# Performance work log

Hardware: AMD Instinct MI355X
Metric: run time of the kernel (lower is better)

Reference implementation:

```python
import jax, jax.numpy as jnp
import numpy as np

B, L, D, H = 2, 4096, 1024, 4
DK = D // H
DV = D // H
CHUNK, FIRS, FIRL, CONV, GROUP = 32, 3, 31, 4, 2
EPS_ID, R_EPS = 0.06, 0.025   # step==0 -> router epsilon at its start value
R_HID = 2 * D
R_IN = D + H * 6


def _l2norm(x, eps=1e-6):
    return x * jax.lax.rsqrt(jnp.sum(x * x, -1, keepdims=True) + eps)


def _causal_dwconv(x, w):
    # x: (b, l, c), w: (c, k); depthwise causal conv1d
    c = x.shape[-1]
    k = w.shape[-1]
    lhs = jnp.swapaxes(x, 1, 2)              # (b, c, l)
    rhs = w[:, None, :]                      # (c, 1, k)
    y = jax.lax.conv_general_dilated(lhs, rhs, window_strides=(1,), padding=[(k - 1, 0)],
                                     dimension_numbers=('NCH', 'OIH', 'NCH'), feature_group_count=c)
    return jnp.swapaxes(y, 1, 2)


def _fir(x, filt):
    # x: (b, l, h, d), filt: (h, d, k) depthwise causal FIR per head-channel
    b, l, h, d = x.shape
    y = _causal_dwconv(x.reshape(b, l, h * d), filt.reshape(h * d, -1))
    return y.reshape(b, l, h, d)


def _delta_rule_chunkwise(q, k, v, beta, chunk=CHUNK):
    # q,k: (b,h,L,dk)  v: (b,h,L,dv)  beta: (b,h,L); L % chunk == 0
    b, h, Ls, dk = q.shape
    dv = v.shape[-1]
    n = Ls // chunk
    q = _l2norm(q)
    k = _l2norm(k)
    v = v * beta[..., None]
    kb = k * beta[..., None]
    rs = lambda t: t.reshape(b, h, n, chunk, -1)
    q, k, v, kb = map(rs, (q, k, v, kb))
    tri = jnp.triu(jnp.ones((chunk, chunk), bool), 0)
    # UT transform: forward substitution to invert (I + strictly-lower(K_beta K^T))
    T = jnp.where(tri, 0.0, -(kb @ jnp.swapaxes(k, -1, -2)))
    for i in range(1, chunk):
        T = T.at[..., i, :].add(jnp.einsum('...j,...jl->...l', T[..., i, :], T))
    T = T + jnp.eye(chunk, dtype=T.dtype)
    u = T @ v          # (b,h,n,c,dv)
    w = T @ kb         # (b,h,n,c,dk)
    fmask = jnp.triu(jnp.ones((chunk, chunk), bool), 1)
    mv = lambda t: jnp.moveaxis(t, 2, 0)

    def step(S, xs):
        qi, ki, ui, wi = xs
        attn = jnp.where(fmask, 0.0, qi @ jnp.swapaxes(ki, -1, -2))
        u2 = ui - wi @ S
        oi = qi @ S + attn @ u2
        return S + jnp.swapaxes(ki, -1, -2) @ u2, oi

    S0 = jnp.zeros((b, h, dk, dv), q.dtype)
    S, o = jax.lax.scan(step, S0, (mv(q), mv(k), mv(u), mv(w)))
    return jnp.moveaxis(o, 0, 2).reshape(b, h, Ls, dv), S


def setup_inputs():
    key = jax.random.key(0)
    ks = jax.random.split(key, 20)
    lin = lambda kk, i, o: 0.02 * jax.random.normal(kk, (i, o), jnp.float32)

    def fir(kk, kern):
        base = jnp.zeros((H, DV, kern), jnp.float32).at[:, :, -1].set(1.0)
        return base + 0.01 * jax.random.normal(kk, (H, DV, kern), jnp.float32)

    return {
        'hidden_states': jax.random.normal(ks[0], (B, L, D), jnp.float32),
        'Wq': lin(ks[1], D, H * DK), 'Wk': lin(ks[2], D, H * DK), 'Wv': lin(ks[3], D, H * DV),
        'Wb': lin(ks[4], D, H),
        'conv_q': 0.3 * jax.random.normal(ks[5], (H * DK, CONV), jnp.float32),
        'conv_k': 0.3 * jax.random.normal(ks[6], (H * DK, CONV), jnp.float32),
        'conv_v': 0.3 * jax.random.normal(ks[7], (H * DV, CONV), jnp.float32),
        'fir_short': fir(ks[8], FIRS), 'fir_long': fir(ks[9], FIRL),
        'alpha_id': jnp.zeros((H,), jnp.float32),
        'Wid': lin(ks[10], D, H), 'bid': jnp.zeros((H,), jnp.float32),
        'Wr1': lin(ks[11], R_IN, R_HID), 'br1': jnp.zeros((R_HID,), jnp.float32),
        'Wr2': lin(ks[12], R_HID, H * 3), 'br2': jnp.zeros((H * 3,), jnp.float32),
        'log_tau_group': jnp.zeros(((H + GROUP - 1) // GROUP,), jnp.float32),
        'log_tau_head': jnp.zeros((H,), jnp.float32),
        'o_norm_w': jnp.ones((DV,), jnp.float32),
        'Wo': lin(ks[13], H * DV, D),
    }


def reference(hidden_states, Wq, Wk, Wv, Wb, conv_q, conv_k, conv_v, fir_short, fir_long,
              alpha_id, Wid, bid, Wr1, br1, Wr2, br2, log_tau_group, log_tau_head, o_norm_w, Wo):
    x = hidden_states
    b, l = x.shape[:2]
    # projections + causal short conv + silu (qk_activation='silu')
    q = jax.nn.silu(_causal_dwconv(x @ Wq, conv_q))
    k = jax.nn.silu(_causal_dwconv(x @ Wk, conv_k))
    v = jax.nn.silu(_causal_dwconv(x @ Wv, conv_v))
    qh = q.reshape(b, l, H, DK)
    kh = k.reshape(b, l, H, DK)
    vh = v.reshape(b, l, H, DV)
    beta = jax.nn.sigmoid(x @ Wb)                      # (b,l,h)
    bhld = lambda t: jnp.transpose(t, (0, 2, 1, 3))
    delta, _S = _delta_rule_chunkwise(bhld(qh), bhld(kh), bhld(vh), jnp.transpose(beta, (0, 2, 1)))
    delta = jnp.transpose(delta, (0, 2, 1, 3))         # (b,l,h,dv)
    fs = _fir(vh, fir_short)
    fl = _fir(vh, fir_long)
    # per-head mean/std stats of the three branch outputs
    stats = jnp.concatenate([fs.mean(-1), fs.std(-1), fl.mean(-1), fl.std(-1),
                             delta.mean(-1), delta.std(-1)], -1)   # (b,l,6h)
    router_in = jnp.concatenate([x, stats], -1)
    hmid = jax.nn.gelu(router_in @ Wr1 + br1, approximate=False)
    logits = (hmid @ Wr2 + br2).reshape(b, l, H, 3)
    group_idx = jnp.arange(H) // GROUP
    # step==0 -> mix=1.0: tau is the per-group temperature
    tau = jnp.exp(log_tau_group)[group_idx] + 0.0 * jnp.exp(log_tau_head)
    p = jax.nn.softmax(logits / tau[None, None, :, None], -1)
    p = p * (1.0 - 3.0 * R_EPS) + R_EPS                # epsilon-floor
    o = p[..., 0:1] * fs + p[..., 1:2] * fl + p[..., 2:3] * delta
    # gated identity (value) path
    id_scale = EPS_ID + jax.nn.sigmoid(alpha_id)[None, None, :] * jax.nn.sigmoid(x @ Wid + bid)
    o = o + id_scale[..., None] * vh
    # per-head RMSNorm then output projection
    o = o * jax.lax.rsqrt(jnp.mean(o * o, -1, keepdims=True) + 1e-5) * o_norm_w
    return o.reshape(b, l, H * DV) @ Wo
```

## Files before the change

### kernel.cpp

```cpp
#include <hip/hip_runtime.h>
#include <hip/hip_bf16.h>
#include <math.h>

#define BATCH 2
#define SEQ 4096
#define DMODEL 1024
#define NH 4
#define DHEAD 256
#define NCHUNK 128
#define ROWS (BATCH * SEQ)

typedef short s8v __attribute__((ext_vector_type(8)));
typedef float f4v __attribute__((ext_vector_type(4)));

__device__ __forceinline__ float sigm(float x) { return 1.0f / (1.0f + expf(-x)); }
__device__ __forceinline__ float siluf(float x) { return x / (1.0f + expf(-x)); }
__device__ __forceinline__ unsigned short f2b(float f) {
  __hip_bfloat16 h = __float2bfloat16(f);
  return *(unsigned short*)&h;
}
__device__ __forceinline__ float b2f(unsigned short u) {
  __hip_bfloat16 h = *(__hip_bfloat16*)&u;
  return __bfloat162float(h);
}

__global__ __launch_bounds__(256) void prep_x(
    const float* __restrict__ x, __hip_bfloat16* __restrict__ xb,
    const float* __restrict__ Wb, const float* __restrict__ Wid,
    const float* __restrict__ alpha_id, const float* __restrict__ bidp,
    float* __restrict__ beta, float* __restrict__ idsc) {
  const int row = blockIdx.x;
  const int t = threadIdx.x;
  const long base = (long)row * DMODEL + t * 4;
  float4 xv = *(const float4*)(x + base);
  {
    __hip_bfloat16 tmp[4] = {__float2bfloat16(xv.x), __float2bfloat16(xv.y),
                             __float2bfloat16(xv.z), __float2bfloat16(xv.w)};
    *(ushort4*)(xb + base) = *(ushort4*)tmp;
  }
  float xa[4] = {xv.x, xv.y, xv.z, xv.w};
  float ab[4] = {0, 0, 0, 0}, ai[4] = {0, 0, 0, 0};
#pragma unroll
  for (int i = 0; i < 4; ++i) {
    int k = t * 4 + i;
    float4 wb4 = *(const float4*)(Wb + k * 4);
    float4 wi4 = *(const float4*)(Wid + k * 4);
    ab[0] = fmaf(xa[i], wb4.x, ab[0]); ab[1] = fmaf(xa[i], wb4.y, ab[1]);
    ab[2] = fmaf(xa[i], wb4.z, ab[2]); ab[3] = fmaf(xa[i], wb4.w, ab[3]);
    ai[0] = fmaf(xa[i], wi4.x, ai[0]); ai[1] = fmaf(xa[i], wi4.y, ai[1]);
    ai[2] = fmaf(xa[i], wi4.z, ai[2]); ai[3] = fmaf(xa[i], wi4.w, ai[3]);
  }
#pragma unroll
  for (int m = 1; m < 64; m <<= 1) {
#pragma unroll
    for (int hh = 0; hh < 4; ++hh) {
      ab[hh] += __shfl_xor(ab[hh], m);
      ai[hh] += __shfl_xor(ai[hh], m);
    }
  }
  __shared__ float red[4][8];
  if ((t & 63) == 0) {
    int wv = t >> 6;
#pragma unroll
    for (int hh = 0; hh < 4; ++hh) {
      red[wv][hh] = ab[hh];
      red[wv][4 + hh] = ai[hh];
    }
  }
  __syncthreads();
  if (t < 8) {
    float s = red[0][t] + red[1][t] + red[2][t] + red[3][t];
    if (t < 4) {
      beta[(long)row * NH + t] = sigm(s);
    } else {
      int hh = t - 4;
      idsc[(long)row * NH + hh] = 0.06f + sigm(alpha_id[hh]) * sigm(s + bidp[hh]);
    }
  }
}

__global__ __launch_bounds__(256) void transpose_cast(
    const float* __restrict__ W, __hip_bfloat16* __restrict__ Wt,
    int K, int N, int Ks) {
  __shared__ float tile[32][33];
  const int t = threadIdx.x;
  const int tx = t & 31, ty = t >> 5;
  const int kb = blockIdx.y * 32, nb = blockIdx.x * 32;
#pragma unroll
  for (int r = 0; r < 4; ++r) {
    int kk = kb + ty + 8 * r;
    tile[ty + 8 * r][tx] = (kk < K) ? W[(long)kk * N + nb + tx] : 0.f;
  }
  __syncthreads();
#pragma unroll
  for (int r = 0; r < 4; ++r) {
    Wt[(long)(nb + ty + 8 * r) * Ks + kb + tx] = __float2bfloat16(tile[tx][ty + 8 * r]);
  }
}

__global__ __launch_bounds__(256) void fir_transpose(
    const float* __restrict__ fshort, const float* __restrict__ flong,
    float* __restrict__ fsT, float* __restrict__ flT) {
  const int j = blockIdx.x;
  const int t = threadIdx.x;
  if (j < 31) {
#pragma unroll
    for (int i = 0; i < 4; ++i) {
      int c = t * 4 + i;
      flT[j * 1024 + c] = flong[c * 31 + j];
    }
  } else {
    int tp = j - 31;
#pragma unroll
    for (int i = 0; i < 4; ++i) {
      int c = t * 4 + i;
      fsT[tp * 1024 + c] = fshort[c * 3 + tp];
    }
  }
}

template <int ACT, bool BF16OUT>
__global__ __launch_bounds__(256) void gemm_bf16(
    const __hip_bfloat16* __restrict__ A, const __hip_bfloat16* __restrict__ Bt,
    const float* __restrict__ bias, void* __restrict__ Cv,
    int M, int N, int Ks) {
  __shared__ short As[128 * 32];
  __shared__ short Bs[128 * 32];
  const int t = threadIdx.x;
  const int wv = t >> 6;
  const int lane = t & 63;
  const int row0 = blockIdx.y * 128, col0 = blockIdx.x * 128;
  const int mq = (wv >> 1) * 64, nq = (wv & 1) * 64;
  const int ln15 = lane & 15;
  const int kq = (lane >> 4) * 8;
  const int sr = t >> 2;
  const int sc = (t & 3) * 8;
  const short* Ag = (const short*)A + (long)(row0 + sr) * Ks + sc;
  const short* Bg = (const short*)Bt + (long)(col0 + sr) * Ks + sc;
  const long rstep = (long)64 * Ks;

  f4v acc[4][4];
#pragma unroll
  for (int i = 0; i < 4; ++i)
#pragma unroll
    for (int j = 0; j < 4; ++j) acc[i][j] = (f4v){0.f, 0.f, 0.f, 0.f};

  uint4 a0 = *(const uint4*)(Ag);
  uint4 a1 = *(const uint4*)(Ag + rstep);
  uint4 b0 = *(const uint4*)(Bg);
  uint4 b1 = *(const uint4*)(Bg + rstep);
// ... 216 lines not shown
#pragma unroll
    for (int i = 0; i < 32; ++i) acc[i] = 0.f;
    for (int j = 0; j < 32; ++j) {
      float vv = v[((long)(b * SEQ + l0 + j)) * DMODEL + h * DHEAD + d];
#pragma unroll
      for (int i = 0; i < 32; ++i) acc[i] = fmaf(T[i][j], vv, acc[i]);
    }
    long ubase = ((long)bh * SEQ + l0) * DHEAD + d;
#pragma unroll
    for (int i = 0; i < 32; ++i) u[ubase + (long)i * DHEAD] = acc[i];
#pragma unroll
    for (int i = 0; i < 32; ++i) acc[i] = 0.f;
    for (int j = 0; j < 32; ++j) {
      float kv = b2f((unsigned short)khi[j * 264 + d]) + b2f((unsigned short)klo[j * 264 + d]);
#pragma unroll
      for (int i = 0; i < 32; ++i) acc[i] = fmaf(T[i][j], kv, acc[i]);
    }
#pragma unroll
    for (int i = 0; i < 32; ++i) wb16[ubase + (long)i * DHEAD] = __float2bfloat16(acc[i]);
  }

  {
    const int s = t;
    unsigned short* kb = (unsigned short*)kTb16 + ((long)bh * NCHUNK + c) * 8192 + (long)s * 32;
#pragma unroll
    for (int i4 = 0; i4 < 8; ++i4) {
      ushort4 pk;
      pk.x = (unsigned short)khi[(i4 * 4 + 0) * 264 + s];
      pk.y = (unsigned short)khi[(i4 * 4 + 1) * 264 + s];
      pk.z = (unsigned short)khi[(i4 * 4 + 2) * 264 + s];
      pk.w = (unsigned short)khi[(i4 * 4 + 3) * 264 + s];
      *(ushort4*)(kb + i4 * 4) = pk;
    }
  }
}

__global__ __launch_bounds__(64, 1) void phaseB(
    const __hip_bfloat16* __restrict__ qpk,
    const __hip_bfloat16* __restrict__ wb,
    const __hip_bfloat16* __restrict__ kTb,
    const __hip_bfloat16* __restrict__ attnb,
    const float* __restrict__ u, float* __restrict__ delta ) {
  __shared__ __align__(16) short St[16 * 264];
  __shared__ __align__(16) short Ut[16 * 40];
  const int bid = blockIdx.x;
  const int slice = bid & 15;
  const int bh = bid >> 4;
  const int d0 = slice * 16;
  const int t = threadIdx.x;
  const int ln15 = t & 15;
  const int qw = t >> 4;

  const short* wbase = (const short*)wb + (long)bh * SEQ * 256;
  const short* qbase = (const short*)qpk + (long)bh * SEQ * 256;
  const short* kTbase = (const short*)kTb + (long)bh * NCHUNK * 8192;
  const short* atbase = (const short*)attnb + (long)bh * NCHUNK * 1024;
  const float* ubase = u + (long)bh * SEQ * 256;
  float* dbase = delta + (long)bh * SEQ * 256;

  f4v Sacc[16];
#pragma unroll
  for (int kt = 0; kt < 16; ++kt) Sacc[kt] = (f4v){0.f, 0.f, 0.f, 0.f};

  s8v wA[2][8], kA[16], atv[2];
  float uf[2][4];
  {
#pragma unroll
    for (int mt = 0; mt < 2; ++mt)
#pragma unroll
      for (int ks = 0; ks < 8; ++ks)
        wA[mt][ks] = *(const s8v*)(wbase + (long)(mt * 16 + ln15) * 256 + ks * 32 + qw * 8);
#pragma unroll
    for (int kt = 0; kt < 16; ++kt)
      kA[kt] = *(const s8v*)(kTbase + (kt * 16 + ln15) * 32 + qw * 8);
#pragma unroll
    for (int mt = 0; mt < 2; ++mt) {
      atv[mt] = *(const s8v*)(atbase + (mt * 16 + ln15) * 32 + qw * 8);
#pragma unroll
      for (int r = 0; r < 4; ++r)
        uf[mt][r] = ubase[(long)(mt * 16 + qw * 4 + r) * 256 + d0 + ln15];
    }
  }

  for (int c = 0; c < NCHUNK; ++c) {
    const int l0 = c * 32;

    s8v qA[2][8];
#pragma unroll
    for (int mt = 0; mt < 2; ++mt)
#pragma unroll
      for (int ks = 0; ks < 8; ++ks)
        qA[mt][ks] = *(const s8v*)(qbase + (long)(l0 + mt * 16 + ln15) * 256 + ks * 32 + qw * 8);

#pragma unroll
    for (int kt = 0; kt < 16; ++kt) {
      ushort4 pk;
      pk.x = f2b(Sacc[kt][0]); pk.y = f2b(Sacc[kt][1]);
      pk.z = f2b(Sacc[kt][2]); pk.w = f2b(Sacc[kt][3]);
      *(ushort4*)&St[ln15 * 264 + kt * 16 + qw * 4] = pk;
    }
    asm volatile("s_waitcnt lgkmcnt(0)" ::: "memory");
    s8v bS[8];
#pragma unroll
    for (int ks = 0; ks < 8; ++ks)
      bS[ks] = *(const s8v*)&St[ln15 * 264 + ks * 32 + qw * 8];

    f4v dwa0 = (f4v){0.f,0.f,0.f,0.f}, dwb0 = (f4v){0.f,0.f,0.f,0.f};
    f4v dwa1 = (f4v){0.f,0.f,0.f,0.f}, dwb1 = (f4v){0.f,0.f,0.f,0.f};
#pragma unroll
    for (int ks = 0; ks < 4; ++ks) {
      dwa0 = __builtin_amdgcn_mfma_f32_16x16x32_bf16(wA[0][ks], bS[ks], dwa0, 0, 0, 0);
      dwa1 = __builtin_amdgcn_mfma_f32_16x16x32_bf16(wA[1][ks], bS[ks], dwa1, 0, 0, 0);
      dwb0 = __builtin_amdgcn_mfma_f32_16x16x32_bf16(wA[0][ks + 4], bS[ks + 4], dwb0, 0, 0, 0);
      dwb1 = __builtin_amdgcn_mfma_f32_16x16x32_bf16(wA[1][ks + 4], bS[ks + 4], dwb1, 0, 0, 0);
    }
    float u2a[4], u2b[4];
#pragma unroll
    for (int r = 0; r < 4; ++r) {
      u2a[r] = uf[0][r] - (dwa0[r] + dwb0[r]);
      u2b[r] = uf[1][r] - (dwa1[r] + dwb1[r]);
    }
    {
      ushort4 pa, pb;
      pa.x = f2b(u2a[0]); pa.y = f2b(u2a[1]); pa.z = f2b(u2a[2]); pa.w = f2b(u2a[3]);
      pb.x = f2b(u2b[0]); pb.y = f2b(u2b[1]); pb.z = f2b(u2b[2]); pb.w = f2b(u2b[3]);
      *(ushort4*)&Ut[ln15 * 40 + qw * 4] = pa;
      *(ushort4*)&Ut[ln15 * 40 + 16 + qw * 4] = pb;
    }
    asm volatile("s_waitcnt lgkmcnt(0)" ::: "memory");
    s8v bu = *(const s8v*)&Ut[ln15 * 40 + qw * 8];

    f4v oA0 = __builtin_amdgcn_mfma_f32_16x16x32_bf16(atv[0], bu, (f4v){0.f,0.f,0.f,0.f}, 0, 0, 0);
    f4v oA1 = __builtin_amdgcn_mfma_f32_16x16x32_bf16(atv[1], bu, (f4v){0.f,0.f,0.f,0.f}, 0, 0, 0);

#pragma unroll
    for (int kt = 0; kt < 16; ++kt)
      Sacc[kt] = __builtin_amdgcn_mfma_f32_16x16x32_bf16(kA[kt], bu, Sacc[kt], 0, 0, 0);

    if (c + 1 < NCHUNK) {
      const int ln = l0 + 32;
#pragma unroll
      for (int mt = 0; mt < 2; ++mt)
#pragma unroll
        for (int ks = 0; ks < 8; ++ks)
          wA[mt][ks] = *(const s8v*)(wbase + (long)(ln + mt * 16 + ln15) * 256 + ks * 32 + qw * 8);
#pragma unroll
      for (int kt = 0; kt < 16; ++kt)
        kA[kt] = *(const s8v*)(kTbase + (long)(c + 1) * 8192 + (kt * 16 + ln15) * 32 + qw * 8);
#pragma unroll
      for (int mt = 0; mt < 2; ++mt) {
        atv[mt] = *(const s8v*)(atbase + (long)(c + 1) * 1024 + (mt * 16 + ln15) * 32 + qw * 8);
#pragma unroll
        for (int r = 0; r < 4; ++r)
          uf[mt][r] = ubase[(long)(ln + mt * 16 + qw * 4 + r) * 256 + d0 + ln15];
      }
    }

    f4v oB0 = (f4v){0.f,0.f,0.f,0.f}, oB1 = (f4v){0.f,0.f,0.f,0.f};
#pragma unroll
    for (int ks = 0; ks < 4; ++ks) {
      oA0 = __builtin_amdgcn_mfma_f32_16x16x32_bf16(qA[0][ks], bS[ks], oA0, 0, 0, 0);
      oA1 = __builtin_amdgcn_mfma_f32_16x16x32_bf16(qA[1][ks], bS[ks], oA1, 0, 0, 0);
      oB0 = __builtin_amdgcn_mfma_f32_16x16x32_bf16(qA[0][ks + 4], bS[ks + 4], oB0, 0, 0, 0);
      oB1 = __builtin_amdgcn_mfma_f32_16x16x32_bf16(qA[1][ks + 4], bS[ks + 4], oB1, 0, 0, 0);
    }
#pragma unroll
    for (int r = 0; r < 4; ++r) {
      dbase[(long)(l0 + qw * 4 + r) * 256 + d0 + ln15] = oA0[r] + oB0[r];
      dbase[(long)(l0 + 16 + qw * 4 + r) * 256 + d0 + ln15] = oA1[r] + oB1[r];
    }
  }
}

__global__ __launch_bounds__(256) void fir_kernel(
    const float* __restrict__ v, const float* __restrict__ fsT,
    const float* __restrict__ flT, float* __restrict__ fs, float* __restrict__ fl) {
  const int row = blockIdx.x;
  const int l = row & (SEQ - 1);
  const int t = threadIdx.x;
  const int cb = t * 4;
  float4 accl = make_float4(0, 0, 0, 0);
  float4 accs = make_float4(0, 0, 0, 0);
  const float* vb = v + (long)(row - 30) * DMODEL + cb;
  if (l >= 30) {
#pragma unroll
    for (int j = 0; j < 31; ++j) {
      float4 w4 = *(const float4*)(flT + j * DMODEL + cb);
      float4 xv = *(const float4*)(vb + (long)j * DMODEL);
      accl.x = fmaf(w4.x, xv.x, accl.x);
      accl.y = fmaf(w4.y, xv.y, accl.y);
      accl.z = fmaf(w4.z, xv.z, accl.z);
      accl.w = fmaf(w4.w, xv.w, accl.w);
      if (j >= 28) {
        float4 s4 = *(const float4*)(fsT + (j - 28) * DMODEL + cb);
        accs.x = fmaf(s4.x, xv.x, accs.x);
        accs.y = fmaf(s4.y, xv.y, accs.y);
        accs.z = fmaf(s4.z, xv.z, accs.z);
        accs.w = fmaf(s4.w, xv.w, accs.w);
      }
    }
  } else {
    for (int j = 30 - l; j < 31; ++j) {
      float4 w4 = *(const float4*)(flT + j * DMODEL + cb);
      float4 xv = *(const float4*)(vb + (long)j * DMODEL);
      accl.x = fmaf(w4.x, xv.x, accl.x);
      accl.y = fmaf(w4.y, xv.y, accl.y);
      accl.z = fmaf(w4.z, xv.z, accl.z);
      accl.w = fmaf(w4.w, xv.w, accl.w);
      if (j >= 28) {
        float4 s4 = *(const float4*)(fsT + (j - 28) * DMODEL + cb);
        accs.x = fmaf(s4.x, xv.x, accs.x);
        accs.y = fmaf(s4.y, xv.y, accs.y);
        accs.z = fmaf(s4.z, xv.z, accs.z);
        accs.w = fmaf(s4.w, xv.w, accs.w);
      }
    }
  }
  *(float4*)(fs + (long)row * DMODEL + cb) = accs;
  *(float4*)(fl + (long)row * DMODEL + cb) = accl;
}

__global__ __launch_bounds__(256) void stats_router(
    const float* __restrict__ x, const float* __restrict__ fs,
    const float* __restrict__ fl, const float* __restrict__ dl,
    __hip_bfloat16* __restrict__ rinb) {
  const int row = blockIdx.x;
  const int b = row >> 12;
  const int l = row & (SEQ - 1);
  const int t = threadIdx.x;
  float4 xv = *(const float4*)(x + (long)row * DMODEL + t * 4);
  {
    __hip_bfloat16 tmp[4] = {__float2bfloat16(xv.x), __float2bfloat16(xv.y),
                             __float2bfloat16(xv.z), __float2bfloat16(xv.w)};
    *(ushort4*)(rinb + (long)row * 1056 + t * 4) = *(ushort4*)tmp;
  }
  if (t < 8) rinb[(long)row * 1056 + 1048 + t] = __float2bfloat16(0.f);
  const int h = t >> 6;
  const int lane = t & 63;
  const long base = (long)row * DMODEL + h * DHEAD + lane * 4;
  const long dbase = ((long)(b * NH + h) * SEQ + l) * DHEAD + lane * 4;
  float4 a = *(const float4*)(fs + base);
  float4 bq = *(const float4*)(fl + base);
  float4 cq = *(const float4*)(dl + dbase);
  float s[6];
  s[0] = a.x + a.y + a.z + a.w;
  s[1] = a.x * a.x + a.y * a.y + a.z * a.z + a.w * a.w;
  s[2] = bq.x + bq.y + bq.z + bq.w;
  s[3] = bq.x * bq.x + bq.y * bq.y + bq.z * bq.z + bq.w * bq.w;
  s[4] = cq.x + cq.y + cq.z + cq.w;
  s[5] = cq.x * cq.x + cq.y * cq.y + cq.z * cq.z + cq.w * cq.w;
#pragma unroll
  for (int m = 1; m < 64; m <<= 1)
#pragma unroll
    for (int j = 0; j < 6; ++j) s[j] += __shfl_xor(s[j], m);
  if (lane == 0) {
    __hip_bfloat16* rb = rinb + (long)row * 1056 + 1024;
    float m0 = s[0] * (1.f / 256.f);
    float m1 = s[2] * (1.f / 256.f);
    float m2 = s[4] * (1.f / 256.f);
    rb[h] = __float2bfloat16(m0);
    rb[4 + h] = __float2bfloat16(sqrtf(fmaxf(s[1] * (1.f / 256.f) - m0 * m0, 0.f)));
    rb[8 + h] = __float2bfloat16(m1);
    rb[12 + h] = __float2bfloat16(sqrtf(fmaxf(s[3] * (1.f / 256.f) - m1 * m1, 0.f)));
    rb[16 + h] = __float2bfloat16(m2);
    rb[20 + h] = __float2bfloat16(sqrtf(fmaxf(s[5] * (1.f / 256.f) - m2 * m2, 0.f)));
  }
}

__global__ __launch_bounds__(256) void router_logits(
    const __hip_bfloat16* __restrict__ hmid, const float* __restrict__ Wr2,
    const float* __restrict__ br2, const float* __restrict__ ltg, float* __restrict__ p) {
  const int row = blockIdx.x;
  const int t = threadIdx.x;
  float acc[12];
#pragma unroll
  for (int j = 0; j < 12; ++j) acc[j] = 0.f;
  const __hip_bfloat16* hr = hmid + (long)row * 2048;
  for (int k = t; k < 2048; k += 256) {
    float hv = __bfloat162float(hr[k]);
    const float* wr = Wr2 + k * 12;
#pragma unroll
    for (int j = 0; j < 12; ++j) acc[j] = fmaf(hv, wr[j], acc[j]);
  }
#pragma unroll
  for (int m = 1; m < 64; m <<= 1)
#pragma unroll
    for (int j = 0; j < 12; ++j) acc[j] += __shfl_xor(acc[j], m);
  __shared__ float red[4][12];
  if ((t & 63) == 0) {
    int wv = t >> 6;
#pragma unroll
    for (int j = 0; j < 12; ++j) red[wv][j] = acc[j];
  }
  __syncthreads();
  if (t < 4) {
    const int h = t;
    float l3[3];
#pragma unroll
// ... 75 lines not shown
  const float* Wo = (const float*)d_in[20];

  float* ws = (float*)d_ws;
  float* pre = ws + 0;
  float* ubuf = ws + 8388608;
  float* wbuf = ws + 16777216;
  float* attnbuf = ws + 25165824;
  float* qbuf = ws + 26214400;
  float* kbuf = ws + 34603008;
  float* vbuf = ws + 42991616;
  float* betabuf = ws + 51380224;
  float* idscbuf = ws + 51412992;
  float* pbuf = ws + 51445760;
  float* flTb = ws + 51544064;
  float* fsTb = ws + 51575808;
  float* deltabuf = ubuf;
  __hip_bfloat16* xb = (__hip_bfloat16*)ubuf;
  __hip_bfloat16* Wqt = (__hip_bfloat16*)(wbuf);
  __hip_bfloat16* Wkt = (__hip_bfloat16*)(wbuf + 524288);
  __hip_bfloat16* Wvt = (__hip_bfloat16*)(wbuf + 1048576);
  __hip_bfloat16* wb16 = (__hip_bfloat16*)wbuf;
  __hip_bfloat16* kTb16 = (__hip_bfloat16*)wbuf + 8388608;
  __hip_bfloat16* attnb16 = (__hip_bfloat16*)attnbuf;
  __hip_bfloat16* qpk16 = (__hip_bfloat16*)pre;
  __hip_bfloat16* rinb = (__hip_bfloat16*)(wbuf);
  __hip_bfloat16* Wr1t = (__hip_bfloat16*)(wbuf + 4325376);
  __hip_bfloat16* Wot = (__hip_bfloat16*)(wbuf + 5406720);
  __hip_bfloat16* omixb = (__hip_bfloat16*)(wbuf);
  __hip_bfloat16* hmid = (__hip_bfloat16*)pre;
  float* fsb = qbuf;
  float* flb = kbuf;

  dim3 blk(256);
  prep_x<<<dim3(ROWS), blk, 0, stream>>>(x, xb, Wb, Wid, alpha_id, bidp, betabuf, idscbuf);
  transpose_cast<<<dim3(32, 32), blk, 0, stream>>>(Wq, Wqt, 1024, 1024, 1024);
  transpose_cast<<<dim3(32, 32), blk, 0, stream>>>(Wk, Wkt, 1024, 1024, 1024);
  transpose_cast<<<dim3(32, 32), blk, 0, stream>>>(Wv, Wvt, 1024, 1024, 1024);
  fir_transpose<<<dim3(34), blk, 0, stream>>>(fir_s, fir_l, fsTb, flTb);
  gemm_bf16<0, false><<<dim3(8, 64), blk, 0, stream>>>(xb, Wqt, nullptr, pre, ROWS, 1024, 1024);
  conv_silu<1><<<dim3(ROWS), blk, 0, stream>>>(pre, conv_q, qbuf);
  gemm_bf16<0, false><<<dim3(8, 64), blk, 0, stream>>>(xb, Wkt, nullptr, pre, ROWS, 1024, 1024);
  conv_silu<1><<<dim3(ROWS), blk, 0, stream>>>(pre, conv_k, kbuf);
  gemm_bf16<0, false><<<dim3(8, 64), blk, 0, stream>>>(xb, Wvt, nullptr, pre, ROWS, 1024, 1024);
  conv_silu<0><<<dim3(ROWS), blk, 0, stream>>>(pre, conv_v, vbuf);
  phaseA<<<dim3(BATCH * NH * NCHUNK), blk, 0, stream>>>(qbuf, kbuf, vbuf, betabuf, ubuf, wb16, kTb16, attnb16, qpk16);
  phaseB<<<dim3(BATCH * NH * 16), dim3(64), 0, stream>>>(qpk16, wb16, kTb16, attnb16, ubuf, deltabuf);
  fir_kernel<<<dim3(ROWS), blk, 0, stream>>>(vbuf, fsTb, flTb, fsb, flb);
  stats_router<<<dim3(ROWS), blk, 0, stream>>>(x, fsb, flb, deltabuf, rinb);
  transpose_cast<<<dim3(64, 33), blk, 0, stream>>>(Wr1, Wr1t, 1048, 2048, 1056);
  transpose_cast<<<dim3(32, 32), blk, 0, stream>>>(Wo, Wot, 1024, 1024, 1024);
  gemm_bf16<1, true><<<dim3(16, 64), blk, 0, stream>>>(rinb, Wr1t, br1, hmid, ROWS, 2048, 1056);
  router_logits<<<dim3(ROWS), blk, 0, stream>>>(hmid, Wr2, br2, ltg, pbuf);
  omix<<<dim3(ROWS), blk, 0, stream>>>(fsb, flb, deltabuf, vbuf, pbuf, idscbuf, onw, omixb);
  gemm_bf16<0, false><<<dim3(8, 64), blk, 0, stream>>>(omixb, Wot, nullptr, d_out, ROWS, 1024, 1024);
}
```

Measured before the change: 851.6 us.

## Merge small launches and co-schedule phaseB recurrence with FIR kernel

Independent prep, weight-transpose and FIR-transpose kernels are merged into one launch using block-index dispatch, and the stats and router/output weight transposes are merged the same way. The sequential phaseB delta-rule scan now packs four waves per block and shares its launch with the FIR convolution blocks at raised priority, so FIR work fills the otherwise idle compute units. The u2 exchange through shared memory is replaced with ds_bpermute lane shuffles. This cuts launch overhead and overlaps a latency-bound serial kernel with bandwidth work, but the FIR blocks may compete with the scan for memory bandwidth and CU slots.

```diff
diff --git a/kernel.cpp b/kernel.cpp
--- a/kernel.cpp
+++ b/kernel.cpp
@@ -23,13 +23,17 @@
   __hip_bfloat16 h = *(__hip_bfloat16*)&u;
   return __bfloat162float(h);
 }
-
-__global__ __launch_bounds__(256) void prep_x(
+__device__ __forceinline__ unsigned int pk2(float lo, float hi) {
+  return (unsigned int)f2b(lo) | ((unsigned int)f2b(hi) << 16);
+}
+
+
+__device__ __forceinline__ void prep_body(
     const float* __restrict__ x, __hip_bfloat16* __restrict__ xb,
     const float* __restrict__ Wb, const float* __restrict__ Wid,
     const float* __restrict__ alpha_id, const float* __restrict__ bidp,
-    float* __restrict__ beta, float* __restrict__ idsc) {
-  const int row = blockIdx.x;
+    float* __restrict__ beta, float* __restrict__ idsc, int row,
+    float (*red)[8]) {
   const int t = threadIdx.x;
   const long base = (long)row * DMODEL + t * 4;
   float4 xv = *(const float4*)(x + base);
@@ -58,7 +62,6 @@
       ai[hh] += __shfl_xor(ai[hh], m);
     }
   }
-  __shared__ float red[4][8];
   if ((t & 63) == 0) {
     int wv = t >> 6;
 #pragma unroll
@@ -79,13 +82,12 @@
   }
 }
 
-__global__ __launch_bounds__(256) void transpose_cast(
+__device__ __forceinline__ void tcast_body(
     const float* __restrict__ W, __hip_bfloat16* __restrict__ Wt,
-    int K, int N, int Ks) {
-  __shared__ float tile[32][33];
+    int K, int N, int Ks, int bx, int by, float (*tile)[33]) {
   const int t = threadIdx.x;
   const int tx = t & 31, ty = t >> 5;
-  const int kb = blockIdx.y * 32, nb = blockIdx.x * 32;
+  const int kb = by * 32, nb = bx * 32;
 #pragma unroll
   for (int r = 0; r < 4; ++r) {
     int kk = kb + ty + 8 * r;
@@ -98,10 +100,9 @@
   }
 }
 
-__global__ __launch_bounds__(256) void fir_transpose(
+__device__ __forceinline__ void firT_body(
     const float* __restrict__ fshort, const float* __restrict__ flong,
-    float* __restrict__ fsT, float* __restrict__ flT) {
-  const int j = blockIdx.x;
+    float* __restrict__ fsT, float* __restrict__ flT, int j) {
   const int t = threadIdx.x;
   if (j < 31) {
 #pragma unroll
@@ -116,6 +117,313 @@
       int c = t * 4 + i;
       fsT[tp * 1024 + c] = fshort[c * 3 + tp];
     }
+  }
+}
+
+__device__ __forceinline__ void fir_body(
+    const float* __restrict__ v, const float* __restrict__ fsT,
+    const float* __restrict__ flT, float* __restrict__ fs, float* __restrict__ fl,
+    int row) {
+  const int l = row & (SEQ - 1);
+  const int t = threadIdx.x;
+  const int cb = t * 4;
+  float4 accl = make_float4(0, 0, 0, 0);
+  float4 accs = make_float4(0, 0, 0, 0);
+  const float* vb = v + (long)(row - 30) * DMODEL + cb;
+  if (l >= 30) {
+#pragma unroll
+    for (int j = 0; j < 31; ++j) {
+      float4 w4 = *(const float4*)(flT + j * DMODEL + cb);
+      float4 xv = *(const float4*)(vb + (long)j * DMODEL);
+      accl.x = fmaf(w4.x, xv.x, accl.x);
+      accl.y = fmaf(w4.y, xv.y, accl.y);
+      accl.z = fmaf(w4.z, xv.z, accl.z);
+      accl.w = fmaf(w4.w, xv.w, accl.w);
+      if (j >= 28) {
+        float4 s4 = *(const float4*)(fsT + (j - 28) * DMODEL + cb);
+        accs.x = fmaf(s4.x, xv.x, accs.x);
+        accs.y = fmaf(s4.y, xv.y, accs.y);
+        accs.z = fmaf(s4.z, xv.z, accs.z);
+        accs.w = fmaf(s4.w, xv.w, accs.w);
+      }
+    }
+  } else {
+    for (int j = 30 - l; j < 31; ++j) {
+      float4 w4 = *(const float4*)(flT + j * DMODEL + cb);
+      float4 xv = *(const float4*)(vb + (long)j * DMODEL);
+      accl.x = fmaf(w4.x, xv.x, accl.x);
+      accl.y = fmaf(w4.y, xv.y, accl.y);
+      accl.z = fmaf(w4.z, xv.z, accl.z);
+      accl.w = fmaf(w4.w, xv.w, accl.w);
+      if (j >= 28) {
+        float4 s4 = *(const float4*)(fsT + (j - 28) * DMODEL + cb);
+        accs.x = fmaf(s4.x, xv.x, accs.x);
+        accs.y = fmaf(s4.y, xv.y, accs.y);
+        accs.z = fmaf(s4.z, xv.z, accs.z);
+        accs.w = fmaf(s4.w, xv.w, accs.w);
+      }
+    }
+  }
+  *(float4*)(fs + (long)row * DMODEL + cb) = accs;
+  *(float4*)(fl + (long)row * DMODEL + cb) = accl;
+}
+
+__device__ __forceinline__ void stats_body(
+    const float* __restrict__ x, const float* __restrict__ fs,
+    const float* __restrict__ fl, const float* __restrict__ dl,
+    __hip_bfloat16* __restrict__ rinb, int row) {
+  const int b = row >> 12;
+  const int l = row & (SEQ - 1);
+  const int t = threadIdx.x;
+  float4 xv = *(const float4*)(x + (long)row * DMODEL + t * 4);
+  {
+    __hip_bfloat16 tmp[4] = {__float2bfloat16(xv.x), __float2bfloat16(xv.y),
+                             __float2bfloat16(xv.z), __float2bfloat16(xv.w)};
+    *(ushort4*)(rinb + (long)row * 1056 + t * 4) = *(ushort4*)tmp;
+  }
+  if (t < 8) rinb[(long)row * 1056 + 1048 + t] = __float2bfloat16(0.f);
+  const int h = t >> 6;
+  const int lane = t & 63;
+  const long base = (long)row * DMODEL + h * DHEAD + lane * 4;
+  const long dbase = ((long)(b * NH + h) * SEQ + l) * DHEAD + lane * 4;
+  float4 a = *(const float4*)(fs + base);
+  float4 bq = *(const float4*)(fl + base);
+  float4 cq = *(const float4*)(dl + dbase);
+  float s[6];
+  s[0] = a.x + a.y + a.z + a.w;
+  s[1] = a.x * a.x + a.y * a.y + a.z * a.z + a.w * a.w;
+  s[2] = bq.x + bq.y + bq.z + bq.w;
+  s[3] = bq.x * bq.x + bq.y * bq.y + bq.z * bq.z + bq.w * bq.w;
+  s[4] = cq.x + cq.y + cq.z + cq.w;
+  s[5] = cq.x * cq.x + cq.y * cq.y + cq.z * cq.z + cq.w * cq.w;
+#pragma unroll
+  for (int m = 1; m < 64; m <<= 1)
+#pragma unroll
+    for (int j = 0; j < 6; ++j) s[j] += __shfl_xor(s[j], m);
+  if (lane == 0) {
+    __hip_bfloat16* rb = rinb + (long)row * 1056 + 1024;
+    float m0 = s[0] * (1.f / 256.f);
+    float m1 = s[2] * (1.f / 256.f);
+    float m2 = s[4] * (1.f / 256.f);
+    rb[h] = __float2bfloat16(m0);
+    rb[4 + h] = __float2bfloat16(sqrtf(fmaxf(s[1] * (1.f / 256.f) - m0 * m0, 0.f)));
+    rb[8 + h] = __float2bfloat16(m1);
+    rb[12 + h] = __float2bfloat16(sqrtf(fmaxf(s[3] * (1.f / 256.f) - m1 * m1, 0.f)));
+    rb[16 + h] = __float2bfloat16(m2);
+    rb[20 + h] = __float2bfloat16(sqrtf(fmaxf(s[5] * (1.f / 256.f) - m2 * m2, 0.f)));
+  }
+}
+
+__device__ __forceinline__ void phaseB_wave(
+    const __hip_bfloat16* __restrict__ qpk, const __hip_bfloat16* __restrict__ wb,
+    const __hip_bfloat16* __restrict__ kTb, const __hip_bfloat16* __restrict__ attnb,
+    const float* __restrict__ u, float* __restrict__ delta,
+    int bh, int d0, short* St, int lane) {
+  const int ln15 = lane & 15;
+  const int qw = (lane >> 4) & 3;
+
+  const short* wbase = (const short*)wb + (long)bh * SEQ * 256;
+  const short* qbase = (const short*)qpk + (long)bh * SEQ * 256;
+  const short* kTbase = (const short*)kTb + (long)bh * NCHUNK * 8192;
+  const short* atbase = (const short*)attnb + (long)bh * NCHUNK * 1024;
+  const float* ubase = u + (long)bh * SEQ * 256;
+  float* dbase = delta + (long)bh * SEQ * 256;
+
+  f4v Sacc[16];
+#pragma unroll
+  for (int kt = 0; kt < 16; ++kt) Sacc[kt] = (f4v){0.f, 0.f, 0.f, 0.f};
+
+  s8v wA[2][8], kA[16], atv[2];
+  float uf[2][4];
+  {
+#pragma unroll
+    for (int mt = 0; mt < 2; ++mt)
+#pragma unroll
+      for (int ks = 0; ks < 8; ++ks)
+        wA[mt][ks] = *(const s8v*)(wbase + (long)(mt * 16 + ln15) * 256 + ks * 32 + qw * 8);
+#pragma unroll
+    for (int kt = 0; kt < 16; ++kt)
+      kA[kt] = *(const s8v*)(kTbase + (kt * 16 + ln15) * 32 + qw * 8);
+#pragma unroll
+    for (int mt = 0; mt < 2; ++mt) {
+      atv[mt] = *(const s8v*)(atbase + (mt * 16 + ln15) * 32 + qw * 8);
+#pragma unroll
+      for (int r = 0; r < 4; ++r)
+        uf[mt][r] = ubase[(long)(mt * 16 + qw * 4 + r) * 256 + d0 + ln15];
+    }
+  }
+
+  const int idx0 = (((qw & 1) * 2) * 16 + ln15) * 4;
+  const int idx1 = (((qw & 1) * 2 + 1) * 16 + ln15) * 4;
+  const bool hiHalf = (qw >= 2);
+
+  for (int c = 0; c < NCHUNK; ++c) {
+    const int l0 = c * 32;
+
+    s8v qA[2][8];
+#pragma unroll
+    for (int mt = 0; mt < 2; ++mt)
+#pragma unroll
+      for (int ks = 0; ks < 8; ++ks)
+        qA[mt][ks] = *(const s8v*)(qbase + (long)(l0 + mt * 16 + ln15) * 256 + ks * 32 + qw * 8);
+
+#pragma unroll
+    for (int kt = 0; kt < 16; ++kt) {
+      ushort4 pk;
+      pk.x = f2b(Sacc[kt][0]); pk.y = f2b(Sacc[kt][1]);
+      pk.z = f2b(Sacc[kt][2]); pk.w = f2b(Sacc[kt][3]);
+      *(ushort4*)&St[ln15 * 264 + kt * 16 + qw * 4] = pk;
+    }
+    asm volatile("s_waitcnt lgkmcnt(0)" ::: "memory");
+    s8v bS[8];
+#pragma unroll
+    for (int ks = 0; ks < 8; ++ks)
+      bS[ks] = *(const s8v*)&St[ln15 * 264 + ks * 32 + qw * 8];
+
+    f4v dwa0 = (f4v){0.f,0.f,0.f,0.f}, dwb0 = (f4v){0.f,0.f,0.f,0.f};
+    f4v dwa1 = (f4v){0.f,0.f,0.f,0.f}, dwb1 = (f4v){0.f,0.f,0.f,0.f};
+#pragma unroll
+    for (int ks = 0; ks < 4; ++ks) {
+      dwa0 = __builtin_amdgcn_mfma_f32_16x16x32_bf16(wA[0][ks], bS[ks], dwa0, 0, 0, 0);
+      dwa1 = __builtin_amdgcn_mfma_f32_16x16x32_bf16(wA[1][ks], bS[ks], dwa1, 0, 0, 0);
+      dwb0 = __builtin_amdgcn_mfma_f32_16x16x32_bf16(wA[0][ks + 4], bS[ks + 4], dwb0, 0, 0, 0);
+      dwb1 = __builtin_amdgcn_mfma_f32_16x16x32_bf16(wA[1][ks + 4], bS[ks + 4], dwb1, 0, 0, 0);
+    }
+    float u2a[4], u2b[4];
+#pragma unroll
+    for (int r = 0; r < 4; ++r) {
+      u2a[r] = uf[0][r] - (dwa0[r] + dwb0[r]);
+      u2b[r] = uf[1][r] - (dwa1[r] + dwb1[r]);
+    }
+    s8v bu;
+    {
+      int A0 = (int)pk2(u2a[0], u2a[1]);
+      int A1 = (int)pk2(u2a[2], u2a[3]);
+      int B0 = (int)pk2(u2b[0], u2b[1]);
+      int B1 = (int)pk2(u2b[2], u2b[3]);
+      int p0a = __builtin_amdgcn_ds_bpermute(idx0, A0);
+      int p0b = __builtin_amdgcn_ds_bpermute(idx0, B0);
+      int p1a = __builtin_amdgcn_ds_bpermute(idx0, A1);
+      int p1b = __builtin_amdgcn_ds_bpermute(idx0, B1);
+      int p2a = __builtin_amdgcn_ds_bpermute(idx1, A0);
+      int p2b = __builtin_amdgcn_ds_bpermute(idx1, B0);
+      int p3a = __builtin_amdgcn_ds_bpermute(idx1, A1);
+      int p3b = __builtin_amdgcn_ds_bpermute(idx1, B1);
+      int4 buw = make_int4(hiHalf ? p0b : p0a, hiHalf ? p1b : p1a,
+                           hiHalf ? p2b : p2a, hiHalf ? p3b : p3a);
+      bu = *(s8v*)&buw;
+    }
+
+    f4v oA0 = __builtin_amdgcn_mfma_f32_16x16x32_bf16(atv[0], bu, (f4v){0.f,0.f,0.f,0.f}, 0, 0, 0);
+    f4v oA1 = __builtin_amdgcn_mfma_f32_16x16x32_bf16(atv[1], bu, (f4v){0.f,0.f,0.f,0.f}, 0, 0, 0);
+
+#pragma unroll
+    for (int kt = 0; kt < 16; ++kt)
+      Sacc[kt] = __builtin_amdgcn_mfma_f32_16x16x32_bf16(kA[kt], bu, Sacc[kt], 0, 0, 0);
+
+    if (c + 1 < NCHUNK) {
+      const int ln = l0 + 32;
+#pragma unroll
+      for (int mt = 0; mt < 2; ++mt)
+#pragma unroll
+        for (int ks = 0; ks < 8; ++ks)
+          wA[mt][ks] = *(const s8v*)(wbase + (long)(ln + mt * 16 + ln15) * 256 + ks * 32 + qw * 8);
+#pragma unroll
+      for (int kt = 0; kt < 16; ++kt)
+        kA[kt] = *(const s8v*)(kTbase + (long)(c + 1) * 8192 + (kt * 16 + ln15) * 32 + qw * 8);
+#pragma unroll
+      for (int mt = 0; mt < 2; ++mt) {
+        atv[mt] = *(const s8v*)(atbase + (long)(c + 1) * 1024 + (mt * 16 + ln15) * 32 + qw * 8);
+#pragma unroll
+        for (int r = 0; r < 4; ++r)
+          uf[mt][r] = ubase[(long)(ln + mt * 16 + qw * 4 + r) * 256 + d0 + ln15];
+      }
+    }
+
+    f4v oB0 = (f4v){0.f,0.f,0.f,0.f}, oB1 = (f4v){0.f,0.f,0.f,0.f};
+#pragma unroll
+    for (int ks = 0; ks < 4; ++ks) {
+      oA0 = __builtin_amdgcn_mfma_f32_16x16x32_bf16(qA[0][ks], bS[ks], oA0, 0, 0, 0);
+      oA1 = __builtin_amdgcn_mfma_f32_16x16x32_bf16(qA[1][ks], bS[ks], oA1, 0, 0, 0);
+      oB0 = __builtin_amdgcn_mfma_f32_16x16x32_bf16(qA[0][ks + 4], bS[ks + 4], oB0, 0, 0, 0);
+      oB1 = __builtin_amdgcn_mfma_f32_16x16x32_bf16(qA[1][ks + 4], bS[ks + 4], oB1, 0, 0, 0);
+    }
+#pragma unroll
+    for (int r = 0; r < 4; ++r) {
+      dbase[(long)(l0 + qw * 4 + r) * 256 + d0 + ln15] = oA0[r] + oB0[r];
+      dbase[(long)(l0 + 16 + qw * 4 + r) * 256 + d0 + ln15] = oA1[r] + oB1[r];
+    }
+  }
+}
+
+
+__global__ __launch_bounds__(256) void head_fused(
+    const float* __restrict__ x, __hip_bfloat16* __restrict__ xb,
+    const float* __restrict__ Wb, const float* __restrict__ Wid,
+    const float* __restrict__ alpha_id, const float* __restrict__ bidp,
+    float* __restrict__ beta, float* __restrict__ idsc,
+    const float* __restrict__ Wq, __hip_bfloat16* __restrict__ Wqt,
+    const float* __restrict__ Wk, __hip_bfloat16* __restrict__ Wkt,
+    const float* __restrict__ Wv, __hip_bfloat16* __restrict__ Wvt,
+    const float* __restrict__ fir_s, const float* __restrict__ fir_l,
+    float* __restrict__ fsT, float* __restrict__ flT) {
+  __shared__ float tile[32][33];
+  __shared__ float red[4][8];
+  const int bid = blockIdx.x;
+  if (bid < 8192) {
+    prep_body(x, xb, Wb, Wid, alpha_id, bidp, beta, idsc, bid, red);
+  } else if (bid < 9216) {
+    int r = bid - 8192;
+    tcast_body(Wq, Wqt, 1024, 1024, 1024, r & 31, r >> 5, tile);
+  } else if (bid < 10240) {
+    int r = bid - 9216;
+    tcast_body(Wk, Wkt, 1024, 1024, 1024, r & 31, r >> 5, tile);
+  } else if (bid < 11264) {
+    int r = bid - 10240;
+    tcast_body(Wv, Wvt, 1024, 1024, 1024, r & 31, r >> 5, tile);
+  } else {
+    firT_body(fir_s, fir_l, fsT, flT, bid - 11264);
+  }
+}
+
+__global__ __launch_bounds__(256, 1) void phaseB_fir(
+    const __hip_bfloat16* __restrict__ qpk, const __hip_bfloat16* __restrict__ wb,
+    const __hip_bfloat16* __restrict__ kTb, const __hip_bfloat16* __restrict__ attnb,
+    const float* __restrict__ u, float* __restrict__ delta,
+    const float* __restrict__ v, const float* __restrict__ fsT,
+    const float* __restrict__ flT, float* __restrict__ fs, float* __restrict__ fl) {
+  __shared__ __align__(16) short Stb[4][16 * 264];
+  const int bid = blockIdx.x;
+  if (bid < 32) {
+    __builtin_amdgcn_s_setprio(1);
+    const int t = threadIdx.x;
+    const int wv = t >> 6;
+    const int lane = t & 63;
+    const int unit = bid * 4 + wv;
+    const int bh = unit >> 4;
+    const int slice = unit & 15;
+    phaseB_wave(qpk, wb, kTb, attnb, u, delta, bh, slice * 16, Stb[wv], lane);
+  } else {
+    fir_body(v, fsT, flT, fs, fl, bid - 32);
+  }
+}
+
+__global__ __launch_bounds__(256) void stats_tcast(
+    const float* __restrict__ x, const float* __restrict__ fs,
+    const float* __restrict__ fl, const float* __restrict__ dl,
+    __hip_bfloat16* __restrict__ rinb,
+    const float* __restrict__ Wr1, __hip_bfloat16* __restrict__ Wr1t,
+    const float* __restrict__ Wo, __hip_bfloat16* __restrict__ Wot) {
+  __shared__ float tile[32][33];
+  const int bid = blockIdx.x;
+  if (bid < 8192) {
+    stats_body(x, fs, fl, dl, rinb, bid);
+  } else if (bid < 10304) {
+    int r = bid - 8192;
+    tcast_body(Wr1, Wr1t, 1048, 2048, 1056, r & 63, r >> 6, tile);
+  } else {
+    int r = bid - 10304;
+    tcast_body(Wo, Wot, 1024, 1024, 1024, r & 31, r >> 5, tile);
   }
 }
 
@@ -398,238 +706,6 @@
       pk.w = (unsigned short)khi[(i4 * 4 + 3) * 264 + s];
       *(ushort4*)(kb + i4 * 4) = pk;
     }
-  }
-}
-
-__global__ __launch_bounds__(64, 1) void phaseB(
-    const __hip_bfloat16* __restrict__ qpk,
-    const __hip_bfloat16* __restrict__ wb,
-    const __hip_bfloat16* __restrict__ kTb,
-    const __hip_bfloat16* __restrict__ attnb,
-    const float* __restrict__ u, float* __restrict__ delta ) {
-  __shared__ __align__(16) short St[16 * 264];
-  __shared__ __align__(16) short Ut[16 * 40];
-  const int bid = blockIdx.x;
-  const int slice = bid & 15;
-  const int bh = bid >> 4;
-  const int d0 = slice * 16;
-  const int t = threadIdx.x;
-  const int ln15 = t & 15;
-  const int qw = t >> 4;
-
-  const short* wbase = (const short*)wb + (long)bh * SEQ * 256;
-  const short* qbase = (const short*)qpk + (long)bh * SEQ * 256;
-  const short* kTbase = (const short*)kTb + (long)bh * NCHUNK * 8192;
-  const short* atbase = (const short*)attnb + (long)bh * NCHUNK * 1024;
-  const float* ubase = u + (long)bh * SEQ * 256;
-  float* dbase = delta + (long)bh * SEQ * 256;
-
-  f4v Sacc[16];
-#pragma unroll
-  for (int kt = 0; kt < 16; ++kt) Sacc[kt] = (f4v){0.f, 0.f, 0.f, 0.f};
-
-  s8v wA[2][8], kA[16], atv[2];
-  float uf[2][4];
-  {
-#pragma unroll
-    for (int mt = 0; mt < 2; ++mt)
-#pragma unroll
-      for (int ks = 0; ks < 8; ++ks)
-        wA[mt][ks] = *(const s8v*)(wbase + (long)(mt * 16 + ln15) * 256 + ks * 32 + qw * 8);
-#pragma unroll
-    for (int kt = 0; kt < 16; ++kt)
-      kA[kt] = *(const s8v*)(kTbase + (kt * 16 + ln15) * 32 + qw * 8);
-#pragma unroll
-    for (int mt = 0; mt < 2; ++mt) {
-      atv[mt] = *(const s8v*)(atbase + (mt * 16 + ln15) * 32 + qw * 8);
-#pragma unroll
-      for (int r = 0; r < 4; ++r)
-        uf[mt][r] = ubase[(long)(mt * 16 + qw * 4 + r) * 256 + d0 + ln15];
-    }
-  }
-
-  for (int c = 0; c < NCHUNK; ++c) {
-    const int l0 = c * 32;
-
-    s8v qA[2][8];
-#pragma unroll
-    for (int mt = 0; mt < 2; ++mt)
-#pragma unroll
-      for (int ks = 0; ks < 8; ++ks)
-        qA[mt][ks] = *(const s8v*)(qbase + (long)(l0 + mt * 16 + ln15) * 256 + ks * 32 + qw * 8);
-
-#pragma unroll
-    for (int kt = 0; kt < 16; ++kt) {
-      ushort4 pk;
-      pk.x = f2b(Sacc[kt][0]); pk.y = f2b(Sacc[kt][1]);
-      pk.z = f2b(Sacc[kt][2]); pk.w = f2b(Sacc[kt][3]);
-      *(ushort4*)&St[ln15 * 264 + kt * 16 + qw * 4] = pk;
-    }
-    asm volatile("s_waitcnt lgkmcnt(0)" ::: "memory");
-    s8v bS[8];
-#pragma unroll
-    for (int ks = 0; ks < 8; ++ks)
-      bS[ks] = *(const s8v*)&St[ln15 * 264 + ks * 32 + qw * 8];
-
-    f4v dwa0 = (f4v){0.f,0.f,0.f,0.f}, dwb0 = (f4v){0.f,0.f,0.f,0.f};
-    f4v dwa1 = (f4v){0.f,0.f,0.f,0.f}, dwb1 = (f4v){0.f,0.f,0.f,0.f};
-#pragma unroll
-    for (int ks = 0; ks < 4; ++ks) {
-      dwa0 = __builtin_amdgcn_mfma_f32_16x16x32_bf16(wA[0][ks], bS[ks], dwa0, 0, 0, 0);
-      dwa1 = __builtin_amdgcn_mfma_f32_16x16x32_bf16(wA[1][ks], bS[ks], dwa1, 0, 0, 0);
-      dwb0 = __builtin_amdgcn_mfma_f32_16x16x32_bf16(wA[0][ks + 4], bS[ks + 4], dwb0, 0, 0, 0);
-      dwb1 = __builtin_amdgcn_mfma_f32_16x16x32_bf16(wA[1][ks + 4], bS[ks + 4], dwb1, 0, 0, 0);
-    }
-    float u2a[4], u2b[4];
-#pragma unroll
-    for (int r = 0; r < 4; ++r) {
-      u2a[r] = uf[0][r] - (dwa0[r] + dwb0[r]);
-      u2b[r] = uf[1][r] - (dwa1[r] + dwb1[r]);
-    }
-    {
-      ushort4 pa, pb;
-      pa.x = f2b(u2a[0]); pa.y = f2b(u2a[1]); pa.z = f2b(u2a[2]); pa.w = f2b(u2a[3]);
-      pb.x = f2b(u2b[0]); pb.y = f2b(u2b[1]); pb.z = f2b(u2b[2]); pb.w = f2b(u2b[3]);
-      *(ushort4*)&Ut[ln15 * 40 + qw * 4] = pa;
-      *(ushort4*)&Ut[ln15 * 40 + 16 + qw * 4] = pb;
-    }
-    asm volatile("s_waitcnt lgkmcnt(0)" ::: "memory");
-    s8v bu = *(const s8v*)&Ut[ln15 * 40 + qw * 8];
-
-    f4v oA0 = __builtin_amdgcn_mfma_f32_16x16x32_bf16(atv[0], bu, (f4v){0.f,0.f,0.f,0.f}, 0, 0, 0);
-    f4v oA1 = __builtin_amdgcn_mfma_f32_16x16x32_bf16(atv[1], bu, (f4v){0.f,0.f,0.f,0.f}, 0, 0, 0);
-
-#pragma unroll
-    for (int kt = 0; kt < 16; ++kt)
-      Sacc[kt] = __builtin_amdgcn_mfma_f32_16x16x32_bf16(kA[kt], bu, Sacc[kt], 0, 0, 0);
-
-    if (c + 1 < NCHUNK) {
-      const int ln = l0 + 32;
-#pragma unroll
-      for (int mt = 0; mt < 2; ++mt)
-#pragma unroll
-        for (int ks = 0; ks < 8; ++ks)
-          wA[mt][ks] = *(const s8v*)(wbase + (long)(ln + mt * 16 + ln15) * 256 + ks * 32 + qw * 8);
-#pragma unroll
-      for (int kt = 0; kt < 16; ++kt)
-        kA[kt] = *(const s8v*)(kTbase + (long)(c + 1) * 8192 + (kt * 16 + ln15) * 32 + qw * 8);
-#pragma unroll
-      for (int mt = 0; mt < 2; ++mt) {
-        atv[mt] = *(const s8v*)(atbase + (long)(c + 1) * 1024 + (mt * 16 + ln15) * 32 + qw * 8);
-#pragma unroll
-        for (int r = 0; r < 4; ++r)
-          uf[mt][r] = ubase[(long)(ln + mt * 16 + qw * 4 + r) * 256 + d0 + ln15];
-      }
-    }
-
-    f4v oB0 = (f4v){0.f,0.f,0.f,0.f}, oB1 = (f4v){0.f,0.f,0.f,0.f};
-#pragma unroll
-    for (int ks = 0; ks < 4; ++ks) {
-      oA0 = __builtin_amdgcn_mfma_f32_16x16x32_bf16(qA[0][ks], bS[ks], oA0, 0, 0, 0);
-      oA1 = __builtin_amdgcn_mfma_f32_16x16x32_bf16(qA[1][ks], bS[ks], oA1, 0, 0, 0);
-      oB0 = __builtin_amdgcn_mfma_f32_16x16x32_bf16(qA[0][ks + 4], bS[ks + 4], oB0, 0, 0, 0);
-      oB1 = __builtin_amdgcn_mfma_f32_16x16x32_bf16(qA[1][ks + 4], bS[ks + 4], oB1, 0, 0, 0);
-    }
-#pragma unroll
-    for (int r = 0; r < 4; ++r) {
-      dbase[(long)(l0 + qw * 4 + r) * 256 + d0 + ln15] = oA0[r] + oB0[r];
-      dbase[(long)(l0 + 16 + qw * 4 + r) * 256 + d0 + ln15] = oA1[r] + oB1[r];
-    }
-  }
-}
-
-__global__ __launch_bounds__(256) void fir_kernel(
-    const float* __restrict__ v, const float* __restrict__ fsT,
-    const float* __restrict__ flT, float* __restrict__ fs, float* __restrict__ fl) {
-  const int row = blockIdx.x;
-  const int l = row & (SEQ - 1);
-  const int t = threadIdx.x;
-  const int cb = t * 4;
-  float4 accl = make_float4(0, 0, 0, 0);
-  float4 accs = make_float4(0, 0, 0, 0);
-  const float* vb = v + (long)(row - 30) * DMODEL + cb;
-  if (l >= 30) {
-#pragma unroll
-    for (int j = 0; j < 31; ++j) {
-      float4 w4 = *(const float4*)(flT + j * DMODEL + cb);
-      float4 xv = *(const float4*)(vb + (long)j * DMODEL);
-      accl.x = fmaf(w4.x, xv.x, accl.x);
-      accl.y = fmaf(w4.y, xv.y, accl.y);
-      accl.z = fmaf(w4.z, xv.z, accl.z);
-      accl.w = fmaf(w4.w, xv.w, accl.w);
-      if (j >= 28) {
-        float4 s4 = *(const float4*)(fsT + (j - 28) * DMODEL + cb);
-        accs.x = fmaf(s4.x, xv.x, accs.x);
-        accs.y = fmaf(s4.y, xv.y, accs.y);
-        accs.z = fmaf(s4.z, xv.z, accs.z);
-        accs.w = fmaf(s4.w, xv.w, accs.w);
-      }
-    }
-  } else {
-    for (int j = 30 - l; j < 31; ++j) {
-      float4 w4 = *(const float4*)(flT + j * DMODEL + cb);
-      float4 xv = *(const float4*)(vb + (long)j * DMODEL);
-      accl.x = fmaf(w4.x, xv.x, accl.x);
-      accl.y = fmaf(w4.y, xv.y, accl.y);
-      accl.z = fmaf(w4.z, xv.z, accl.z);
-      accl.w = fmaf(w4.w, xv.w, accl.w);
-      if (j >= 28) {
-        float4 s4 = *(const float4*)(fsT + (j - 28) * DMODEL + cb);
-        accs.x = fmaf(s4.x, xv.x, accs.x);
-        accs.y = fmaf(s4.y, xv.y, accs.y);
-        accs.z = fmaf(s4.z, xv.z, accs.z);
-        accs.w = fmaf(s4.w, xv.w, accs.w);
-      }
-    }
-  }
-  *(float4*)(fs + (long)row * DMODEL + cb) = accs;
-  *(float4*)(fl + (long)row * DMODEL + cb) = accl;
-}
-
-__global__ __launch_bounds__(256) void stats_router(
-    const float* __restrict__ x, const float* __restrict__ fs,
-    const float* __restrict__ fl, const float* __restrict__ dl,
-    __hip_bfloat16* __restrict__ rinb) {
-  const int row = blockIdx.x;
-  const int b = row >> 12;
-  const int l = row & (SEQ - 1);
-  const int t = threadIdx.x;
-  float4 xv = *(const float4*)(x + (long)row * DMODEL + t * 4);
-  {
-    __hip_bfloat16 tmp[4] = {__float2bfloat16(xv.x), __float2bfloat16(xv.y),
-                             __float2bfloat16(xv.z), __float2bfloat16(xv.w)};
-    *(ushort4*)(rinb + (long)row * 1056 + t * 4) = *(ushort4*)tmp;
-  }
-  if (t < 8) rinb[(long)row * 1056 + 1048 + t] = __float2bfloat16(0.f);
-  const int h = t >> 6;
-  const int lane = t & 63;
-  const long base = (long)row * DMODEL + h * DHEAD + lane * 4;
-  const long dbase = ((long)(b * NH + h) * SEQ + l) * DHEAD + lane * 4;
-  float4 a = *(const float4*)(fs + base);
-  float4 bq = *(const float4*)(fl + base);
-  float4 cq = *(const float4*)(dl + dbase);
-  float s[6];
-  s[0] = a.x + a.y + a.z + a.w;
-  s[1] = a.x * a.x + a.y * a.y + a.z * a.z + a.w * a.w;
-  s[2] = bq.x + bq.y + bq.z + bq.w;
-  s[3] = bq.x * bq.x + bq.y * bq.y + bq.z * bq.z + bq.w * bq.w;
-  s[4] = cq.x + cq.y + cq.z + cq.w;
-  s[5] = cq.x * cq.x + cq.y * cq.y + cq.z * cq.z + cq.w * cq.w;
-#pragma unroll
-  for (int m = 1; m < 64; m <<= 1)
-#pragma unroll
-    for (int j = 0; j < 6; ++j) s[j] += __shfl_xor(s[j], m);
-  if (lane == 0) {
-    __hip_bfloat16* rb = rinb + (long)row * 1056 + 1024;
-    float m0 = s[0] * (1.f / 256.f);
-    float m1 = s[2] * (1.f / 256.f);
-    float m2 = s[4] * (1.f / 256.f);
-    rb[h] = __float2bfloat16(m0);
-    rb[4 + h] = __float2bfloat16(sqrtf(fmaxf(s[1] * (1.f / 256.f) - m0 * m0, 0.f)));
-    rb[8 + h] = __float2bfloat16(m1);
-    rb[12 + h] = __float2bfloat16(sqrtf(fmaxf(s[3] * (1.f / 256.f) - m1 * m1, 0.f)));
-    rb[16 + h] = __float2bfloat16(m2);
-    rb[20 + h] = __float2bfloat16(sqrtf(fmaxf(s[5] * (1.f / 256.f) - m2 * m2, 0.f)));
   }
 }
 
@@ -771,11 +847,8 @@
   float* flb = kbuf;
 
   dim3 blk(256);
-  prep_x<<<dim3(ROWS), blk, 0, stream>>>(x, xb, Wb, Wid, alpha_id, bidp, betabuf, idscbuf);
-  transpose_cast<<<dim3(32, 32), blk, 0, stream>>>(Wq, Wqt, 1024, 1024, 1024);
-  transpose_cast<<<dim3(32, 32), blk, 0, stream>>>(Wk, Wkt, 1024, 1024, 1024);
-  transpose_cast<<<dim3(32, 32), blk, 0, stream>>>(Wv, Wvt, 1024, 1024, 1024);
-  fir_transpose<<<dim3(34), blk, 0, stream>>>(fir_s, fir_l, fsTb, flTb);
+  head_fused<<<dim3(11298), blk, 0, stream>>>(x, xb, Wb, Wid, alpha_id, bidp,
+      betabuf, idscbuf, Wq, Wqt, Wk, Wkt, Wv, Wvt, fir_s, fir_l, fsTb, flTb);
   gemm_bf16<0, false><<<dim3(8, 64), blk, 0, stream>>>(xb, Wqt, nullptr, pre, ROWS, 1024, 1024);
   conv_silu<1><<<dim3(ROWS), blk, 0, stream>>>(pre, conv_q, qbuf);
   gemm_bf16<0, false><<<dim3(8, 64), blk, 0, stream>>>(xb, Wkt, nullptr, pre, ROWS, 1024, 1024);
@@ -783,11 +856,9 @@
   gemm_bf16<0, false><<<dim3(8, 64), blk, 0, stream>>>(xb, Wvt, nullptr, pre, ROWS, 1024, 1024);
   conv_silu<0><<<dim3(ROWS), blk, 0, stream>>>(pre, conv_v, vbuf);
   phaseA<<<dim3(BATCH * NH * NCHUNK), blk, 0, stream>>>(qbuf, kbuf, vbuf, betabuf, ubuf, wb16, kTb16, attnb16, qpk16);
-  phaseB<<<dim3(BATCH * NH * 16), dim3(64), 0, stream>>>(qpk16, wb16, kTb16, attnb16, ubuf, deltabuf);
-  fir_kernel<<<dim3(ROWS), blk, 0, stream>>>(vbuf, fsTb, flTb, fsb, flb);
-  stats_router<<<dim3(ROWS), blk, 0, stream>>>(x, fsb, flb, deltabuf, rinb);
-  transpose_cast<<<dim3(64, 33), blk, 0, stream>>>(Wr1, Wr1t, 1048, 2048, 1056);
-  transpose_cast<<<dim3(32, 32), blk, 0, stream>>>(Wo, Wot, 1024, 1024, 1024);
+  phaseB_fir<<<dim3(32 + ROWS), blk, 0, stream>>>(qpk16, wb16, kTb16, attnb16, ubuf, deltabuf,
+      vbuf, fsTb, flTb, fsb, flb);
+  stats_tcast<<<dim3(11328), blk, 0, stream>>>(x, fsb, flb, deltabuf, rinb, Wr1, Wr1t, Wo, Wot);
   gemm_bf16<1, true><<<dim3(16, 64), blk, 0, stream>>>(rinb, Wr1t, br1, hmid, ROWS, 2048, 1056);
   router_logits<<<dim3(ROWS), blk, 0, stream>>>(hmid, Wr2, br2, ltg, pbuf);
   omix<<<dim3(ROWS), blk, 0, stream>>>(fsb, flb, deltabuf, vbuf, pbuf, idscbuf, onw, omixb);
```

After: 1.174 ms. +37.8%, slower.
